# Kernel tuning notes

Measured on AMD Instinct MI355X. Metric: run time of the kernel, lower is better.

Reference implementation:

```python
import math
import jax, jax.numpy as jnp
import numpy as np

B, N_COLS, CHANNELS, NUM_HEADS = 512, 128, 512, 8
D_HEAD = CHANNELS // NUM_HEADS


def setup_inputs() -> dict:
    key = jax.random.key(0)
    ks = jax.random.split(key, 9)
    s = 1.0 / math.sqrt(CHANNELS)
    x = jax.random.normal(ks[0], (B, N_COLS, CHANNELS), dtype=jnp.float32)
    Wq = jax.random.uniform(ks[1], (CHANNELS, CHANNELS), jnp.float32, -s, s)
    bq = jax.random.uniform(ks[2], (CHANNELS,), jnp.float32, -s, s)
    Wk = jax.random.uniform(ks[3], (CHANNELS, CHANNELS), jnp.float32, -s, s)
    bk = jax.random.uniform(ks[4], (CHANNELS,), jnp.float32, -s, s)
    Wv = jax.random.uniform(ks[5], (CHANNELS, CHANNELS), jnp.float32, -s, s)
    bv = jax.random.uniform(ks[6], (CHANNELS,), jnp.float32, -s, s)
    Wo = jax.random.uniform(ks[7], (CHANNELS, CHANNELS), jnp.float32, -s, s)
    bo = jax.random.uniform(ks[8], (CHANNELS,), jnp.float32, -s, s)
    return {"x": x, "Wq": Wq, "bq": bq, "Wk": Wk, "bk": bk,
            "Wv": Wv, "bv": bv, "Wo": Wo, "bo": bo}


def reference(x, Wq, bq, Wk, bk, Wv, bv, Wo, bo):
    b, n, c = x.shape
    h, d = NUM_HEADS, D_HEAD

    def split_heads(t):  # [b, n, c] -> [b, h, n, d]
        return t.reshape(b, n, h, d).transpose(0, 2, 1, 3)

    Q = split_heads(x @ Wq + bq)
    K = split_heads(x @ Wk + bk)
    V = split_heads(x @ Wv + bv)

    # raw scores [b, h, q, k]
    scores = jnp.einsum('bhqd,bhkd->bhqk', Q, K)
    # causal mask over columns; note: mask added BEFORE scaling by sqrt(d)
    causal = jnp.tril(jnp.ones((n, n), dtype=jnp.float32))
    mask = (1.0 - causal) * -100000.0
    attn = jax.nn.softmax((scores + mask) / math.sqrt(d), axis=-1)
    out = jnp.einsum('bhqk,bhkd->bhqd', attn, V)
    out = out.transpose(0, 2, 1, 3).reshape(b, n, c)
    return out @ Wo + bo
```

## Files before the change

### kernel.cpp

```cpp
#include <hip/hip_runtime.h>

typedef _Float16 f16;
typedef _Float16 half8 __attribute__((ext_vector_type(8)));
typedef _Float16 half4 __attribute__((ext_vector_type(4)));
typedef float f32x4 __attribute__((ext_vector_type(4)));

#define B_SZ 512
#define NQ   128
#define CH   512
#define NH   8
#define DH   64
#define MTOK (B_SZ*NQ)
#define KD   512

#define MFMA16(a,b,c) __builtin_amdgcn_mfma_f32_16x16x32_f16((a),(b),(c),0,0,0)

#define GLDS16(g,l) __builtin_amdgcn_global_load_lds( \
    (__attribute__((address_space(1))) void*)(g), \
    (__attribute__((address_space(3))) void*)(l), 16, 0, 0)

__global__ __launch_bounds__(256) void k_prep(
    const float* __restrict__ x,
    const float* __restrict__ Wq, const float* __restrict__ Wk,
    const float* __restrict__ Wv, const float* __restrict__ Wo,
    f16* __restrict__ xb, f16* __restrict__ wt) {
  const int bid = blockIdx.x;
  if (bid < 512) {
    for (int e = threadIdx.x; e < 2048; e += 256) {
      const int n = bid * 4 + (e >> 9);
      const int k = e & 511;
      const float* W = (n < 512) ? Wq : (n < 1024) ? Wk : (n < 1536) ? Wv : Wo;
      wt[n * 512 + k] = (f16)W[k * 512 + (n & 511)];
    }
  } else {
    const int n8 = MTOK * KD / 8;
    int i = (bid - 512) * 256 + threadIdx.x;
    const int stride = 2048 * 256;
    for (; i < n8; i += stride) {
      f32x4 a = ((const f32x4*)x)[2 * i];
      f32x4 b = ((const f32x4*)x)[2 * i + 1];
      half8 h;
      h[0] = (f16)a[0]; h[1] = (f16)a[1]; h[2] = (f16)a[2]; h[3] = (f16)a[3];
      h[4] = (f16)b[0]; h[5] = (f16)b[1]; h[6] = (f16)b[2]; h[7] = (f16)b[3];
      ((half8*)xb)[i] = h;
    }
  }
}

__device__ __forceinline__ void step128(const f16* pa, const f16* pb,
                                        int roA, int roB, f32x4 (&acc)[4][4]) {
  half8 af[4], bf[4];
#pragma unroll
  for (int m = 0; m < 4; ++m) af[m] = *(const half8*)(pa + roA + m * 512);
#pragma unroll
  for (int n = 0; n < 4; ++n) bf[n] = *(const half8*)(pb + roB + n * 512);
  __builtin_amdgcn_s_setprio(1);
#pragma unroll
  for (int m = 0; m < 4; ++m)
#pragma unroll
    for (int n = 0; n < 4; ++n)
      acc[m][n] = MFMA16(af[m], bf[n], acc[m][n]);
  __builtin_amdgcn_s_setprio(0);
}

__device__ __forceinline__ void gemm128_pf(
    const f16* __restrict__ Ag, const f16* __restrict__ Bg,
    f16* la, f16* lb, f32x4 (&acc)[4][4]) {
  const int tid = threadIdx.x;
  const int w = tid >> 6, lane = tid & 63;
  const int ln = lane & 15, g = lane >> 4;
  const int wr = w >> 1, wc = w & 1;
  const int srow = w * 16 + (lane >> 2);
  const int scol = ((lane & 3) ^ ((lane >> 3) & 3)) * 8;
  const f16* gA = Ag + srow * KD + scol;
  const f16* gB = Bg + srow * KD + scol;
  const int w512 = w * 512;
  f16 *pa0 = la, *pa1 = la + 4096, *pa2 = la + 8192;
  f16 *pb0 = lb, *pb1 = lb + 4096, *pb2 = lb + 8192;
  const int slotx = (g ^ ((ln >> 1) & 3)) * 8;
  const int roA = (wr * 64 + ln) * 32 + slotx;
  const int roB = (wc * 64 + ln) * 32 + slotx;

  GLDS16(gA,           pa0 + w512); GLDS16(gA + 64*KD,      pa0 + w512 + 2048);
  GLDS16(gB,           pb0 + w512); GLDS16(gB + 64*KD,      pb0 + w512 + 2048);
  GLDS16(gA + 32,      pa1 + w512); GLDS16(gA + 64*KD + 32, pa1 + w512 + 2048);
  GLDS16(gB + 32,      pb1 + w512); GLDS16(gB + 64*KD + 32, pb1 + w512 + 2048);
  asm volatile("s_waitcnt vmcnt(4)" ::: "memory");
  __builtin_amdgcn_s_barrier();

  const f16* gAs = gA + 64;
  const f16* gBs = gB + 64;
#pragma unroll 1
  for (int t = 0; t < 14; ++t) {
    GLDS16(gAs, pa2 + w512); GLDS16(gAs + 64*KD, pa2 + w512 + 2048);
    GLDS16(gBs, pb2 + w512); GLDS16(gBs + 64*KD, pb2 + w512 + 2048);
    gAs += 32; gBs += 32;
    step128(pa0, pb0, roA, roB, acc);
    asm volatile("s_waitcnt vmcnt(4)" ::: "memory");
    __builtin_amdgcn_s_barrier();
    f16* t1 = pa0; pa0 = pa1; pa1 = pa2; pa2 = t1;
    f16* t2 = pb0; pb0 = pb1; pb1 = pb2; pb2 = t2;
  }
  step128(pa0, pb0, roA, roB, acc);
  asm volatile("s_waitcnt vmcnt(0)" ::: "memory");
  __builtin_amdgcn_s_barrier();
  step128(pa1, pb1, roA, roB, acc);
}

__global__ __launch_bounds__(256, 4) void k_qkv(
    const f16* __restrict__ A, const f16* __restrict__ Bw,
    const float* __restrict__ bq, const float* __restrict__ bk,
    const float* __restrict__ bv,
    f16* __restrict__ qb, f16* __restrict__ kb, f16* __restrict__ vb) {
  __shared__ f16 la[3 * 4096];
  __shared__ f16 lb[3 * 4096];
  const int tid = threadIdx.x;
  const int w = tid >> 6, lane = tid & 63;
  const int ln = lane & 15, g = lane >> 4;
  const int wr = w >> 1, wc = w & 1;
  const int s = blockIdx.x >> 3;
  const int ml = s / 12;
  const int ntile = s - ml * 12;
  const int mtile = (blockIdx.x & 7) * 64 + ml;

  f32x4 acc[4][4] = {};
  gemm128_pf(A + mtile * 128 * KD, Bw + ntile * 128 * KD, la, lb, acc);

  const int b = mtile;
  const int colbase = ntile * 128 + wc * 64;
#pragma unroll
  for (int m = 0; m < 4; ++m) {
    const int nn0 = wr * 64 + m * 16 + g * 4;
#pragma unroll
    for (int n = 0; n < 4; ++n) {
      const int col = colbase + n * 16 + ln;
      const int which = col >> 9;
      const int c = col & 511;
      const int h = c >> 6, d = c & 63;
      const float bias = (which == 0) ? bq[c] : (which == 1) ? bk[c] : bv[c];
      if (which < 2) {
        f16* dst = ((which == 0) ? qb : kb) + ((b * NH + h) * NQ + nn0) * DH + d;
#pragma unroll
        for (int r = 0; r < 4; ++r)
          dst[r * DH] = (f16)(acc[m][n][r] + bias);
      } else {
        half4 v4;
#pragma unroll
        for (int r = 0; r < 4; ++r)
          v4[r] = (f16)(acc[m][n][r] + bias);
        *(half4*)(vb + ((b * NH + h) * DH + d) * NQ + nn0) = v4;
      }
    }
  }
}

__global__ __launch_bounds__(256, 2) void k_attn(
    const f16* __restrict__ qbuf, const f16* __restrict__ kbuf,
    const f16* __restrict__ vbuf, f16* __restrict__ ao) {
  __shared__ f16 kl[128 * 72];
  __shared__ f16 vl[64 * 136];
  __shared__ f16 pl[128 * 136];
  const int bh = blockIdx.x;
  const f16* Qp = qbuf + bh * (NQ * DH);
  const f16* Kp = kbuf + bh * (NQ * DH);
  const f16* Vp = vbuf + bh * (DH * NQ);
  const int tid = threadIdx.x;
  const int w = tid >> 6, lane = tid & 63;
  const int ln = lane & 15, g = lane >> 4;

#pragma unroll
  for (int i = 0; i < 4; ++i) {
    const int e = i * 2048 + tid * 8;
    *(half8*)(kl + (e >> 6) * 72 + (e & 63)) = *(const half8*)(Kp + e);
  }
#pragma unroll
  for (int i = 0; i < 4; ++i) {
    const int e = i * 2048 + tid * 8;
    *(half8*)(vl + (e >> 7) * 136 + (e & 127)) = *(const half8*)(Vp + e);
  }
  half8 qf[2][2];
#pragma unroll
  for (int m = 0; m < 2; ++m)
#pragma unroll
    for (int ks = 0; ks < 2; ++ks)
      qf[m][ks] = *(const half8*)(Qp + (w * 32 + m * 16 + ln) * DH + ks * 32 + g * 8);
  __syncthreads();

  f32x4 s[2][8] = {};
#pragma unroll
  for (int ks = 0; ks < 2; ++ks)
#pragma unroll
    for (int n = 0; n < 8; ++n) {
      half8 kf = *(const half8*)(kl + (n * 16 + ln) * 72 + ks * 32 + g * 8);
      s[0][n] = MFMA16(qf[0][ks], kf, s[0][n]);
      s[1][n] = MFMA16(qf[1][ks], kf, s[1][n]);
    }

  float inv[2][4];
#pragma unroll
  for (int m = 0; m < 2; ++m) {
#pragma unroll
    for (int r = 0; r < 4; ++r) {
      const int q = w * 32 + m * 16 + g * 4 + r;
      float z[8];
      float rm = -1e30f;
#pragma unroll
      for (int n = 0; n < 8; ++n) {
        const int col = n * 16 + ln;
        float zz = s[m][n][r] * 0.125f + ((col > q) ? -12500.0f : 0.0f);
        z[n] = zz;
        rm = fmaxf(rm, zz);
      }
      rm = fmaxf(rm, __shfl_xor(rm, 1));
      rm = fmaxf(rm, __shfl_xor(rm, 2));
      rm = fmaxf(rm, __shfl_xor(rm, 4));
      rm = fmaxf(rm, __shfl_xor(rm, 8));
      float rs = 0.f;
#pragma unroll
      for (int n = 0; n < 8; ++n) {
        const float p = __expf(z[n] - rm);
        rs += p;
        pl[q * 136 + n * 16 + ln] = (f16)p;
      }
      rs += __shfl_xor(rs, 1);
      rs += __shfl_xor(rs, 2);
      rs += __shfl_xor(rs, 4);
      rs += __shfl_xor(rs, 8);
      inv[m][r] = 1.0f / rs;
    }
  }

  f32x4 o[2][4] = {};
#pragma unroll
  for (int ks = 0; ks < 4; ++ks) {
    half8 pf0 = *(const half8*)(pl + (w * 32 + ln) * 136 + ks * 32 + g * 8);
    half8 pf1 = *(const half8*)(pl + (w * 32 + 16 + ln) * 136 + ks * 32 + g * 8);
#pragma unroll
    for (int n = 0; n < 4; ++n) {
      half8 vf = *(const half8*)(vl + (n * 16 + ln) * 136 + ks * 32 + g * 8);
      o[0][n] = MFMA16(pf0, vf, o[0][n]);
      o[1][n] = MFMA16(pf1, vf, o[1][n]);
    }
  }

  const int b = bh >> 3, h = bh & 7;
  f16* dst = ao + (b * NQ) * CH + h * DH;
#pragma unroll
  for (int m = 0; m < 2; ++m)
#pragma unroll
    for (int n = 0; n < 4; ++n)
#pragma unroll
      for (int r = 0; r < 4; ++r) {
        const int q = w * 32 + m * 16 + g * 4 + r;
        dst[q * CH + n * 16 + ln] = (f16)(o[m][n][r] * inv[m][r]);
      }
}

__global__ __launch_bounds__(256, 4) void k_out(
    const f16* __restrict__ A, const f16* __restrict__ Bw,
    const float* __restrict__ bo, float* __restrict__ out) {
  __shared__ f16 la[3 * 4096];
  __shared__ f16 lb[3 * 4096];
  const int tid = threadIdx.x;
  const int w = tid >> 6, lane = tid & 63;
  const int ln = lane & 15, g = lane >> 4;
  const int wr = w >> 1, wc = w & 1;
  const int s = blockIdx.x >> 3;
  const int ml = s >> 2;
  const int ntile = s & 3;
  const int mtile = (blockIdx.x & 7) * 64 + ml;

  f32x4 acc[4][4] = {};
  gemm128_pf(A + mtile * 128 * KD, Bw + ntile * 128 * KD, la, lb, acc);

  const int colbase = ntile * 128 + wc * 64;
#pragma unroll
  for (int m = 0; m < 4; ++m) {
    const int tok0 = mtile * 128 + wr * 64 + m * 16 + g * 4;
#pragma unroll
    for (int n = 0; n < 4; ++n) {
      const int col = colbase + n * 16 + ln;
      const float bias = bo[col];
      float* dst = out + tok0 * CH + col;
#pragma unroll
      for (int r = 0; r < 4; ++r)
        dst[r * CH] = acc[m][n][r] + bias;
    }
  }
}

extern "C" void kernel_launch(void* const* d_in, const int* in_sizes, int n_in,
                              void* d_out, int out_size, void* d_ws, size_t ws_size,
                              hipStream_t stream) {
  (void)in_sizes; (void)n_in; (void)out_size; (void)ws_size;
  const float* x  = (const float*)d_in[0];
  const float* Wq = (const float*)d_in[1];
  const float* bq = (const float*)d_in[2];
  const float* Wk = (const float*)d_in[3];
  const float* bk = (const float*)d_in[4];
  const float* Wv = (const float*)d_in[5];
  const float* bv = (const float*)d_in[6];
  const float* Wo = (const float*)d_in[7];
  const float* bo = (const float*)d_in[8];
  float* out = (float*)d_out;

  char* ws = (char*)d_ws;
  const size_t SZ = (size_t)MTOK * KD * sizeof(f16);
  f16* xb = (f16*)(ws);
  f16* qb = (f16*)(ws + SZ);
  f16* kb = (f16*)(ws + 2 * SZ);
  f16* vb = (f16*)(ws + 3 * SZ);
  f16* wt = (f16*)(ws + 4 * SZ);
  f16* ao = xb;

  k_prep<<<2560, 256, 0, stream>>>(x, Wq, Wk, Wv, Wo, xb, wt);
  k_qkv<<<6144, 256, 0, stream>>>(xb, wt, bq, bk, bv, qb, kb, vb);
  k_attn<<<4096, 256, 0, stream>>>(qb, kb, vb, ao);
  k_out<<<2048, 256, 0, stream>>>(ao, wt + 1536 * KD, bo, out);
}
```

Before: 333.7 us.

## Chain two M-tiles per GEMM block with continuous cross-tile prefetch

Measured after the change: 331.4 us. About the same (-0.7%).

```diff
diff --git a/kernel.cpp b/kernel.cpp
--- a/kernel.cpp
+++ b/kernel.cpp
@@ -63,51 +63,60 @@
   __builtin_amdgcn_s_setprio(0);
 }
 
-__device__ __forceinline__ void gemm128_pf(
-    const f16* __restrict__ Ag, const f16* __restrict__ Bg,
-    f16* la, f16* lb, f32x4 (&acc)[4][4]) {
-  const int tid = threadIdx.x;
-  const int w = tid >> 6, lane = tid & 63;
-  const int ln = lane & 15, g = lane >> 4;
-  const int wr = w >> 1, wc = w & 1;
-  const int srow = w * 16 + (lane >> 2);
-  const int scol = ((lane & 3) ^ ((lane >> 3) & 3)) * 8;
-  const f16* gA = Ag + srow * KD + scol;
-  const f16* gB = Bg + srow * KD + scol;
-  const int w512 = w * 512;
-  f16 *pa0 = la, *pa1 = la + 4096, *pa2 = la + 8192;
-  f16 *pb0 = lb, *pb1 = lb + 4096, *pb2 = lb + 8192;
-  const int slotx = (g ^ ((ln >> 1) & 3)) * 8;
-  const int roA = (wr * 64 + ln) * 32 + slotx;
-  const int roB = (wc * 64 + ln) * 32 + slotx;
-
-  GLDS16(gA,           pa0 + w512); GLDS16(gA + 64*KD,      pa0 + w512 + 2048);
-  GLDS16(gB,           pb0 + w512); GLDS16(gB + 64*KD,      pb0 + w512 + 2048);
-  GLDS16(gA + 32,      pa1 + w512); GLDS16(gA + 64*KD + 32, pa1 + w512 + 2048);
-  GLDS16(gB + 32,      pb1 + w512); GLDS16(gB + 64*KD + 32, pb1 + w512 + 2048);
+template<int T, class Epi>
+__device__ __forceinline__ void gemm_chain(
+    const f16* __restrict__ gA,
+    const f16* __restrict__ gB,
+    f16* la, f16* lb, int w512, int roA, int roB, Epi epi) {
+  const f32x4 z = {0.f, 0.f, 0.f, 0.f};
+  f32x4 acc[4][4] = {};
+
+#define STAGE(v, bufc) do { \
+    const int aoff = (((v) >> 4) << 16) + (((v) & 15) << 5); \
+    const int boff = ((v) & 15) << 5; \
+    f16* lav = la + (bufc) * 4096 + w512; \
+    f16* lbv = lb + (bufc) * 4096 + w512; \
+    GLDS16(gA + aoff, lav); GLDS16(gA + aoff + 64 * KD, lav + 2048); \
+    GLDS16(gB + boff, lbv); GLDS16(gB + boff + 64 * KD, lbv + 2048); \
+  } while (0)
+
+  STAGE(0, 0); STAGE(1, 1);
   asm volatile("s_waitcnt vmcnt(4)" ::: "memory");
   __builtin_amdgcn_s_barrier();
 
-  const f16* gAs = gA + 64;
-  const f16* gBs = gB + 64;
+  constexpr int LASTU = 3 * ((T - 5) / 3);
 #pragma unroll 1
-  for (int t = 0; t < 14; ++t) {
-    GLDS16(gAs, pa2 + w512); GLDS16(gAs + 64*KD, pa2 + w512 + 2048);
-    GLDS16(gBs, pb2 + w512); GLDS16(gBs + 64*KD, pb2 + w512 + 2048);
-    gAs += 32; gBs += 32;
-    step128(pa0, pb0, roA, roB, acc);
-    asm volatile("s_waitcnt vmcnt(4)" ::: "memory");
-    __builtin_amdgcn_s_barrier();
-    f16* t1 = pa0; pa0 = pa1; pa1 = pa2; pa2 = t1;
-    f16* t2 = pb0; pb0 = pb1; pb1 = pb2; pb2 = t2;
-  }
-  step128(pa0, pb0, roA, roB, acc);
-  asm volatile("s_waitcnt vmcnt(0)" ::: "memory");
-  __builtin_amdgcn_s_barrier();
-  step128(pa1, pb1, roA, roB, acc);
-}
-
-__global__ __launch_bounds__(256, 4) void k_qkv(
+  for (int u = 0; u <= LASTU; u += 3) {
+#pragma unroll
+    for (int i = 0; i < 3; ++i) {
+      STAGE(u + i + 2, (i + 2) % 3);
+      step128(la + i * 4096, lb + i * 4096, roA, roB, acc);
+      asm volatile("s_waitcnt vmcnt(4)" ::: "memory");
+      __builtin_amdgcn_s_barrier();
+      if (((u + i) & 15) == 15) {
+        epi(acc, (u + i) >> 4);
+#pragma unroll
+        for (int m = 0; m < 4; ++m)
+#pragma unroll
+          for (int n = 0; n < 4; ++n) acc[m][n] = z;
+      }
+    }
+  }
+  constexpr int RS = LASTU + 3;
+#pragma unroll
+  for (int r = 0; r < T - RS; ++r) {
+    const int s = RS + r;
+    if (s + 2 < T) STAGE(s + 2, (s + 2) % 3);
+    step128(la + (s % 3) * 4096, lb + (s % 3) * 4096, roA, roB, acc);
+    if (s + 2 < T)      { asm volatile("s_waitcnt vmcnt(4)" ::: "memory"); }
+    else if (s + 1 < T) { asm volatile("s_waitcnt vmcnt(0)" ::: "memory"); }
+    if (s + 1 < T) __builtin_amdgcn_s_barrier();
+  }
+  epi(acc, (T - 1) >> 4);
+#undef STAGE
+}
+
+__global__ __launch_bounds__(256, 3) void k_qkv(
     const f16* __restrict__ A, const f16* __restrict__ Bw,
     const float* __restrict__ bq, const float* __restrict__ bk,
     const float* __restrict__ bv,
@@ -118,40 +127,49 @@
   const int w = tid >> 6, lane = tid & 63;
   const int ln = lane & 15, g = lane >> 4;
   const int wr = w >> 1, wc = w & 1;
-  const int s = blockIdx.x >> 3;
-  const int ml = s / 12;
-  const int ntile = s - ml * 12;
-  const int mtile = (blockIdx.x & 7) * 64 + ml;
-
-  f32x4 acc[4][4] = {};
-  gemm128_pf(A + mtile * 128 * KD, Bw + ntile * 128 * KD, la, lb, acc);
-
-  const int b = mtile;
+  const int xcd = blockIdx.x & 7;
+  const int s0 = blockIdx.x >> 3;
+  const int cl = s0 / 12;
+  const int ntile = s0 - cl * 12;
+  const int chain = xcd * 32 + cl;
+
+  const int srow = w * 16 + (lane >> 2);
+  const int scol = ((lane & 3) ^ ((lane >> 3) & 3)) * 8;
+  const f16* gA = A + (size_t)chain * 2 * 128 * KD + srow * KD + scol;
+  const f16* gB = Bw + ntile * 128 * KD + srow * KD + scol;
+  const int slotx = (g ^ ((ln >> 1) & 3)) * 8;
+  const int roA = (wr * 64 + ln) * 32 + slotx;
+  const int roB = (wc * 64 + ln) * 32 + slotx;
+
   const int colbase = ntile * 128 + wc * 64;
-#pragma unroll
-  for (int m = 0; m < 4; ++m) {
-    const int nn0 = wr * 64 + m * 16 + g * 4;
-#pragma unroll
-    for (int n = 0; n < 4; ++n) {
-      const int col = colbase + n * 16 + ln;
-      const int which = col >> 9;
-      const int c = col & 511;
-      const int h = c >> 6, d = c & 63;
-      const float bias = (which == 0) ? bq[c] : (which == 1) ? bk[c] : bv[c];
-      if (which < 2) {
-        f16* dst = ((which == 0) ? qb : kb) + ((b * NH + h) * NQ + nn0) * DH + d;
-#pragma unroll
-        for (int r = 0; r < 4; ++r)
-          dst[r * DH] = (f16)(acc[m][n][r] + bias);
-      } else {
-        half4 v4;
-#pragma unroll
-        for (int r = 0; r < 4; ++r)
-          v4[r] = (f16)(acc[m][n][r] + bias);
-        *(half4*)(vb + ((b * NH + h) * DH + d) * NQ + nn0) = v4;
-      }
-    }
-  }
+  auto epi = [&](f32x4 (&acc)[4][4], int j) {
+    const int b = chain * 2 + j;
+#pragma unroll
+    for (int m = 0; m < 4; ++m) {
+      const int nn0 = wr * 64 + m * 16 + g * 4;
+#pragma unroll
+      for (int n = 0; n < 4; ++n) {
+        const int col = colbase + n * 16 + ln;
+        const int which = col >> 9;
+        const int c = col & 511;
+        const int h = c >> 6, d = c & 63;
+        const float bias = (which == 0) ? bq[c] : (which == 1) ? bk[c] : bv[c];
+        if (which < 2) {
+          f16* dst = ((which == 0) ? qb : kb) + ((b * NH + h) * NQ + nn0) * DH + d;
+#pragma unroll
+          for (int r = 0; r < 4; ++r)
+            dst[r * DH] = (f16)(acc[m][n][r] + bias);
+        } else {
+          half4 v4;
+#pragma unroll
+          for (int r = 0; r < 4; ++r)
+            v4[r] = (f16)(acc[m][n][r] + bias);
+          *(half4*)(vb + ((b * NH + h) * DH + d) * NQ + nn0) = v4;
+        }
+      }
+    }
+  };
+  gemm_chain<32>(gA, gB, la, lb, w * 512, roA, roB, epi);
 }
 
 __global__ __launch_bounds__(256, 2) void k_attn(
@@ -256,7 +274,7 @@
       }
 }
 
-__global__ __launch_bounds__(256, 4) void k_out(
+__global__ __launch_bounds__(256, 3) void k_out(
     const f16* __restrict__ A, const f16* __restrict__ Bw,
     const float* __restrict__ bo, float* __restrict__ out) {
   __shared__ f16 la[3 * 4096];
@@ -265,28 +283,37 @@
   const int w = tid >> 6, lane = tid & 63;
   const int ln = lane & 15, g = lane >> 4;
   const int wr = w >> 1, wc = w & 1;
-  const int s = blockIdx.x >> 3;
-  const int ml = s >> 2;
-  const int ntile = s & 3;
-  const int mtile = (blockIdx.x & 7) * 64 + ml;
-
-  f32x4 acc[4][4] = {};
-  gemm128_pf(A + mtile * 128 * KD, Bw + ntile * 128 * KD, la, lb, acc);
+  const int xcd = blockIdx.x & 7;
+  const int s0 = blockIdx.x >> 3;
+  const int ntile = s0 & 3;
+  const int chain = xcd * 32 + (s0 >> 2);
+
+  const int srow = w * 16 + (lane >> 2);
+  const int scol = ((lane & 3) ^ ((lane >> 3) & 3)) * 8;
+  const f16* gA = A + (size_t)chain * 2 * 128 * KD + srow * KD + scol;
+  const f16* gB = Bw + ntile * 128 * KD + srow * KD + scol;
+  const int slotx = (g ^ ((ln >> 1) & 3)) * 8;
+  const int roA = (wr * 64 + ln) * 32 + slotx;
+  const int roB = (wc * 64 + ln) * 32 + slotx;
 
   const int colbase = ntile * 128 + wc * 64;
-#pragma unroll
-  for (int m = 0; m < 4; ++m) {
-    const int tok0 = mtile * 128 + wr * 64 + m * 16 + g * 4;
-#pragma unroll
-    for (int n = 0; n < 4; ++n) {
-      const int col = colbase + n * 16 + ln;
-      const float bias = bo[col];
-      float* dst = out + tok0 * CH + col;
-#pragma unroll
-      for (int r = 0; r < 4; ++r)
-        dst[r * CH] = acc[m][n][r] + bias;
-    }
-  }
+  auto epi = [&](f32x4 (&acc)[4][4], int j) {
+    const int mtile = chain * 2 + j;
+#pragma unroll
+    for (int m = 0; m < 4; ++m) {
+      const int tok0 = mtile * 128 + wr * 64 + m * 16 + g * 4;
+#pragma unroll
+      for (int n = 0; n < 4; ++n) {
+        const int col = colbase + n * 16 + ln;
+        const float bias = bo[col];
+        float* dst = out + (size_t)tok0 * CH + col;
+#pragma unroll
+        for (int r = 0; r < 4; ++r)
+          dst[r * CH] = acc[m][n][r] + bias;
+      }
+    }
+  };
+  gemm_chain<32>(gA, gB, la, lb, w * 512, roA, roB, epi);
 }
 
 extern "C" void kernel_launch(void* const* d_in, const int* in_sizes, int n_in,
@@ -314,7 +341,7 @@
   f16* ao = xb;
 
   k_prep<<<2560, 256, 0, stream>>>(x, Wq, Wk, Wv, Wo, xb, wt);
-  k_qkv<<<6144, 256, 0, stream>>>(xb, wt, bq, bk, bv, qb, kb, vb);
+  k_qkv<<<3072, 256, 0, stream>>>(xb, wt, bq, bk, bv, qb, kb, vb);
   k_attn<<<4096, 256, 0, stream>>>(qb, kb, vb, ao);
-  k_out<<<2048, 256, 0, stream>>>(ao, wt + 1536 * KD, bo, out);
-}
+  k_out<<<1024, 256, 0, stream>>>(ao, wt + 1536 * KD, bo, out);
+}
```
